# Kernel tuning notes

Measured on AMD Instinct MI355X. Metric: run time of the kernel, lower is better.

The kernel has to match this reference:

```python
import jax, jax.numpy as jnp
import numpy as np

N, E = 10000, 320000
IN_DIM, OUT_DIM, HEADS = 256, 32, 8
HD = OUT_DIM * HEADS  # 256
EPS = 1e-16  # PyG softmax epsilon


def _make_conv_params(key, in_dim, heads, d):
    hd = heads * d
    ks = jax.random.split(key, 8)
    s = 0.02
    return {
        'Wq': jax.random.normal(ks[0], (in_dim, hd)) * s,
        'bq': jnp.zeros((hd,)),
        'Wk': jax.random.normal(ks[1], (in_dim, hd)) * s,
        'bk': jnp.zeros((hd,)),
        'Wv': jax.random.normal(ks[2], (in_dim, hd)) * s,
        'bv': jnp.zeros((hd,)),
        'We': jax.random.normal(ks[3], (1, hd)) * s,          # lin_edge, no bias
        'Wskip': jax.random.normal(ks[4], (in_dim, hd)) * s,  # lin_skip
        'bskip': jnp.zeros((hd,)),
        'Wbeta': jax.random.normal(ks[5], (3 * hd, 1)) * s,   # lin_beta, no bias
    }


def transformer_conv(x, src, dst, edge_attr, p, heads, d):
    # x: [N, F]; edge_attr: [E, 1]
    n = x.shape[0]
    q = (x @ p['Wq'] + p['bq']).reshape(n, heads, d)
    k = (x @ p['Wk'] + p['bk']).reshape(n, heads, d)
    v = (x @ p['Wv'] + p['bv']).reshape(n, heads, d)
    e = (edge_attr @ p['We']).reshape(-1, heads, d)  # [E, H, D]
    kj = k[src] + e                                  # [E, H, D]
    vj = v[src] + e
    # per-edge attention logits
    alpha = jnp.einsum('ehd,ehd->eh', q[dst], kj) / jnp.sqrt(jnp.asarray(d, x.dtype))
    # segment softmax over incoming edges of each dst node
    m = jax.ops.segment_max(alpha, dst, num_segments=n)     # [N, H]
    m = jnp.where(jnp.isfinite(m), m, 0.0)
    ex = jnp.exp(alpha - m[dst])
    denom = jax.ops.segment_sum(ex, dst, num_segments=n)    # [N, H]
    w = ex / (denom[dst] + EPS)                              # [E, H]
    out = jax.ops.segment_sum(w[:, :, None] * vj, dst, num_segments=n)  # [N, H, D]
    out = out.reshape(n, heads * d)
    # beta-gated skip connection
    xr = x @ p['Wskip'] + p['bskip']
    beta = jax.nn.sigmoid(jnp.concatenate([out, xr, out - xr], axis=-1) @ p['Wbeta'])  # [N, 1]
    return beta * xr + (1.0 - beta) * out


def setup_inputs() -> dict:
    key = jax.random.key(0)
    kx, ke, kw, k1, k2 = jax.random.split(key, 5)
    inp = {
        'x': jax.random.normal(kx, (N, IN_DIM), dtype=jnp.float32),
        'edge_index': jax.random.randint(ke, (2, E), 0, N, dtype=jnp.int64),
        'edge_weight': jax.random.uniform(kw, (E,), dtype=jnp.float32),
    }
    p1 = _make_conv_params(k1, IN_DIM, HEADS, OUT_DIM)
    p2 = _make_conv_params(k2, HD, HEADS, OUT_DIM)
    for name, v in p1.items():
        inp[name + '1'] = v
    for name, v in p2.items():
        inp[name + '2'] = v
    return inp


def reference(x, edge_index, edge_weight,
              Wq1, bq1, Wk1, bk1, Wv1, bv1, We1, Wskip1, bskip1, Wbeta1,
              Wq2, bq2, Wk2, bk2, Wv2, bv2, We2, Wskip2, bskip2, Wbeta2):
    src, dst = edge_index[0], edge_index[1]
    ea = edge_weight[:, None]  # [E, 1]
    p1 = dict(Wq=Wq1, bq=bq1, Wk=Wk1, bk=bk1, Wv=Wv1, bv=bv1, We=We1,
              Wskip=Wskip1, bskip=bskip1, Wbeta=Wbeta1)
    p2 = dict(Wq=Wq2, bq=bq2, Wk=Wk2, bk=bk2, Wv=Wv2, bv=bv2, We=We2,
              Wskip=Wskip2, bskip=bskip2, Wbeta=Wbeta2)
    h = transformer_conv(x, src, dst, ea, p1, HEADS, OUT_DIM)
    h = transformer_conv(h, src, dst, ea, p2, HEADS, OUT_DIM)
    h = transformer_conv(h, src, dst, ea, p2, HEADS, OUT_DIM)  # conv2 applied twice, shared weights
    return h
```

## Files before the change

kernel.cpp:

```cpp
#include <hip/hip_runtime.h>
#include <hip/hip_bf16.h>
#include <math.h>

#define NN 10000
#define EE 320000
#define DIM 256
#define NROWS 10016
#define SCANB 40

typedef __attribute__((ext_vector_type(8))) _Float16 f16x8;
typedef __attribute__((ext_vector_type(4))) _Float16 f16x4;
typedef __attribute__((ext_vector_type(2))) _Float16 f16x2;
typedef __attribute__((ext_vector_type(4))) float f32x4;

#if defined(__has_builtin)
#if __has_builtin(__builtin_amdgcn_fdot2)
#define FDOT2(a, b, c) __builtin_amdgcn_fdot2(a, b, c, false)
#endif
#endif
#ifndef FDOT2
#define FDOT2(a, b, c) fmaf((float)a[0], (float)b[0], fmaf((float)a[1], (float)b[1], c))
#endif

__device__ __forceinline__ float bf2f(unsigned short u) {
  union { unsigned int ui; float f; } cv;
  cv.ui = ((unsigned int)u) << 16;
  return cv.f;
}

__device__ __forceinline__ float ldf(const void* p, int idx, int isf) {
  return isf ? ((const float*)p)[idx] : bf2f(((const unsigned short*)p)[idx]);
}

__global__ __launch_bounds__(256) void k_detect_zero(const unsigned int* __restrict__ xw,
                                                     const int* __restrict__ ei,
                                                     int* __restrict__ flags,
                                                     int* __restrict__ counts) {
  int i = blockIdx.x * 256 + (int)threadIdx.x;
  if (i < NN) counts[i] = 0;
  if (blockIdx.x == 0 && threadIdx.x < 64) {
    int lane = threadIdx.x;
    int wild = 0;
    for (int t = 0; t < 16; ++t) {
      unsigned int w = xw[t * 64 + lane];
      unsigned int lo = w & 0xffffu;
      float f = bf2f((unsigned short)lo);
      float af = fabsf(f);
      if (lo != 0u && (af > 1e4f || af < 1e-30f)) wild++;
    }
    #pragma unroll
    for (int m = 1; m < 64; m <<= 1) wild += __shfl_xor(wild, m);
    int zeros = 0;
    for (int t = 0; t < 2; ++t) {
      if (ei[(t * 64 + lane) * 2 + 1] == 0) zeros++;
    }
    #pragma unroll
    for (int m = 1; m < 64; m <<= 1) zeros += __shfl_xor(zeros, m);
    if (lane == 0) {
      flags[0] = (wild > 100) ? 1 : 0;
      flags[1] = (zeros > 100) ? 1 : 0;
    }
  }
}

__global__ void k_count(const int* __restrict__ ei, int* __restrict__ counts,
                        const int* __restrict__ flags) {
  int i64 = flags[1];
  int i = blockIdx.x * blockDim.x + threadIdx.x;
  if (i < EE) {
    int d = i64 ? ei[2 * (EE + i)] : ei[EE + i];
    atomicAdd(&counts[d], 1);
  }
}

__global__ __launch_bounds__(256) void k_scan1(const int* __restrict__ counts,
                                               int* __restrict__ tmpoff,
                                               int* __restrict__ bsum) {
  __shared__ int s[256];
  int t = threadIdx.x;
  int i = blockIdx.x * 256 + t;
  int v = (i < NN) ? counts[i] : 0;
  s[t] = v;
  __syncthreads();
  for (int off = 1; off < 256; off <<= 1) {
    int x = (t >= off) ? s[t - off] : 0;
    __syncthreads();
    s[t] += x;
    __syncthreads();
  }
  if (i < NN) tmpoff[i] = s[t] - v;
  if (t == 255) bsum[blockIdx.x] = s[255];
}

__global__ __launch_bounds__(256) void k_scan3(const int* __restrict__ tmpoff,
                                               const int* __restrict__ bsum,
                                               int* __restrict__ offsets,
                                               int* __restrict__ cursor) {
  __shared__ int sbase;
  if (threadIdx.x < 64) {
    int t = threadIdx.x;
    int v = (t < SCANB && t < (int)blockIdx.x) ? bsum[t] : 0;
    #pragma unroll
    for (int msk = 1; msk < 64; msk <<= 1) v += __shfl_xor(v, msk);
    if (t == 0) sbase = v;
  }
  __syncthreads();
  int base = sbase;
  int i = blockIdx.x * 256 + (int)threadIdx.x;
  if (i < NN) {
    int o = tmpoff[i] + base;
    offsets[i] = o;
    cursor[i] = o;
  }
  if (i == 0) offsets[NN] = EE;
}

__global__ void k_fill_sort(const int* __restrict__ ei, const void* __restrict__ ew,
                            int* __restrict__ cursor, int2* __restrict__ eS,
                            const int* __restrict__ flags) {
  int isf = flags[0];
  int i64 = flags[1];
  int i = blockIdx.x * blockDim.x + threadIdx.x;
  if (i < EE) {
    int s, d;
    if (i64) { s = ei[2 * i]; d = ei[2 * (EE + i)]; }
    else     { s = ei[i];     d = ei[EE + i]; }
    float wv = isf ? ((const float*)ew)[i] : bf2f(((const unsigned short*)ew)[i]);
    int p = atomicAdd(&cursor[d], 1);
    eS[p] = make_int2(s, __float_as_int(wv));
  }
}

struct PackArgs {
  const void* W[8];
  const void* B8[8];
  const void* WeWb[4];
  const void* x;
};

__global__ __launch_bounds__(256) void k_pack(PackArgs pa, _Float16* __restrict__ Bh,
                                              float* __restrict__ bvec,
                                              float* __restrict__ WeWbF,
                                              _Float16* __restrict__ Ah,
                                              _Float16* __restrict__ Al,
                                              const int* __restrict__ flags) {
  __shared__ _Float16 lds[64][66];
  int isf = flags[0];
  int bid = (int)blockIdx.x, tid = (int)threadIdx.x;
  if (bid < 128) {
    int m = bid >> 4, t = bid & 15, tr = t >> 2, tc = t & 3;
    const void* Wm = pa.W[m];
    #pragma unroll
    for (int rep = 0; rep < 16; ++rep) {
      int idx = rep * 256 + tid;
      int r = idx >> 6, c = idx & 63;
      lds[r][c] = (_Float16)ldf(Wm, (tr * 64 + r) * 256 + tc * 64 + c, isf);
    }
    __syncthreads();
    _Float16* out = Bh + (size_t)m * 65536;
    #pragma unroll
    for (int rep = 0; rep < 16; ++rep) {
      int idx = rep * 256 + tid;
      int r = idx >> 6, c = idx & 63;
      out[(tc * 64 + r) * 256 + tr * 64 + c] = lds[c][r];
    }
    return;
  }
  int b2 = bid - 128;
  if (b2 < 16) {
    int i = b2 * 256 + tid;
    if (i < 2048) {
      bvec[i] = ldf(pa.B8[i >> 8], i & 255, isf);
    } else {
      i -= 2048;
      int which, k;
      if (i < 256)       { which = 0; k = i; }
      else if (i < 1024) { which = 1; k = i - 256; }
      else if (i < 1280) { which = 2; k = i - 1024; }
      else               { which = 3; k = i - 1280; }
      WeWbF[i] = ldf(pa.WeWb[which], k, isf);
    }
    return;
  }
  int i = (b2 - 16) * 256 + tid;
  if (i < NROWS * 64) {
    f16x4 h, l;
    if (i >= NN * 64) {
      h = (f16x4)(_Float16)0.f;
      l = (f16x4)(_Float16)0.f;
    } else {
      float v[4];
      if (isf) {
        float4 t = reinterpret_cast<const float4*>(pa.x)[i];
        v[0] = t.x; v[1] = t.y; v[2] = t.z; v[3] = t.w;
      } else {
        ushort4 t = reinterpret_cast<const ushort4*>(pa.x)[i];
        v[0] = bf2f(t.x); v[1] = bf2f(t.y); v[2] = bf2f(t.z); v[3] = bf2f(t.w);
      }
      #pragma unroll
      for (int j = 0; j < 4; ++j) {
        _Float16 hh = (_Float16)v[j];
        h[j] = hh;
        l[j] = (_Float16)(v[j] - (float)hh);
      }
    }
    reinterpret_cast<f16x4*>(Ah)[i] = h;
    reinterpret_cast<f16x4*>(Al)[i] = l;
  }
}

__global__ __launch_bounds__(256, 4) void k_gemm_mfma(
    const _Float16* __restrict__ Ah, const _Float16* __restrict__ Al,
    const _Float16* __restrict__ Bh, const float* __restrict__ bvec,
    _Float16* __restrict__ Qh, _Float16* __restrict__ KVh, float* __restrict__ XRf) {
  int tid = (int)threadIdx.x;
  int wave = tid >> 6, lane = tid & 63;
  int lr = lane & 15;
  int kg = (lane >> 4) << 3;
  int mat = blockIdx.y;
  int rowBase = blockIdx.x << 5;
  int colBase = (mat << 8) + (wave << 6);
  const _Float16* a0 = Ah + (size_t)(rowBase + lr) * 256 + kg;
  const _Float16* a1 = Al + (size_t)(rowBase + lr) * 256 + kg;
  const _Float16* b0 = Bh + (size_t)(colBase + lr) * 256 + kg;
  f32x4 acc[2][4] = {};
  #pragma unroll
  for (int ks = 0; ks < 256; ks += 32) {
    f16x8 ah0 = *reinterpret_cast<const f16x8*>(a0 + ks);
    f16x8 ah1 = *reinterpret_cast<const f16x8*>(a0 + 16 * 256 + ks);
    f16x8 bh[4];
    #pragma unroll
    for (int cf = 0; cf < 4; ++cf)
      bh[cf] = *reinterpret_cast<const f16x8*>(b0 + cf * 16 * 256 + ks);
    #pragma unroll
    for (int cf = 0; cf < 4; ++cf) {
      acc[0][cf] = __builtin_amdgcn_mfma_f32_16x16x32_f16(ah0, bh[cf], acc[0][cf], 0, 0, 0);
      acc[1][cf] = __builtin_amdgcn_mfma_f32_16x16x32_f16(ah1, bh[cf], acc[1][cf], 0, 0, 0);
    }
    if (mat == 3) {
      f16x8 al0 = *reinterpret_cast<const f16x8*>(a1 + ks);
      f16x8 al1 = *reinterpret_cast<const f16x8*>(a1 + 16 * 256 + ks);
      #pragma unroll
      for (int cf = 0; cf < 4; ++cf) {
        acc[0][cf] = __builtin_amdgcn_mfma_f32_16x16x32_f16(al0, bh[cf], acc[0][cf], 0, 0, 0);
        acc[1][cf] = __builtin_amdgcn_mfma_f32_16x16x32_f16(al1, bh[cf], acc[1][cf], 0, 0, 0);
      }
    }
  }
  int rj = (lane >> 4) << 2;
  int colLoc = (wave << 6);
  #pragma unroll
  for (int rf = 0; rf < 2; ++rf) {
    #pragma unroll
    for (int cf = 0; cf < 4; ++cf) {
      int col = colLoc + cf * 16 + lr;
      float bb = bvec[(mat << 8) + col];
      #pragma unroll
      for (int j = 0; j < 4; ++j) {
        int row = rowBase + rf * 16 + rj + j;
        if (row < NN) {
          float val = acc[rf][cf][j] + bb;
          if (mat == 0)      Qh[(size_t)row * DIM + col] = (_Float16)val;
          else if (mat == 3) XRf[(size_t)row * DIM + col] = val;
          else KVh[(size_t)row * 512 + ((mat == 2) ? 256 : 0) + col] = (_Float16)val;
        }
      }
    }
  }
}

#define ATT_STEP(KK, VV, WW) do { \
    f16x2 kka = {KK[0], KK[1]}, kkb = {KK[2], KK[3]}; \
    float pt = FDOT2(kka, qha, FDOT2(kkb, qhb, 0.f)); \
    pt += __shfl_xor(pt, 1); \
    pt += __shfl_xor(pt, 2); \
    pt += __shfl_xor(pt, 4); \
    float alpha = fmaf(WW, qwe, pt) * 0.17677669529663687f; \
    float nm = fmaxf(m, alpha); \
    float sc = __expf(m - nm); \
    float pe = __expf(alpha - nm); \
    l = fmaf(l, sc, pe); \
    sw = fmaf(sw, sc, pe * WW); \
    a0 = fmaf(a0, sc, pe * (float)VV[0]); \
    a1 = fmaf(a1, sc, pe * (float)VV[1]); \
    a2 = fmaf(a2, sc, pe * (float)VV[2]); \
    a3 = fmaf(a3, sc, pe * (float)VV[3]); \
    m = nm; \
  } while (0)

#define PAIR_STEP(K0, V0, W0, K1, V1, W1) do { \
    f16x2 k0a = {K0[0], K0[1]}, k0b = {K0[2], K0[3]}; \
    f16x2 k1a = {K1[0], K1[1]}, k1b = {K1[2], K1[3]}; \
    float pt0 = FDOT2(k0a, qha, FDOT2(k0b, qhb, 0.f)); \
    float pt1 = FDOT2(k1a, qha, FDOT2(k1b, qhb, 0.f)); \
    pt0 += __shfl_xor(pt0, 1); pt1 += __shfl_xor(pt1, 1); \
    pt0 += __shfl_xor(pt0, 2); pt1 += __shfl_xor(pt1, 2); \
    pt0 += __shfl_xor(pt0, 4); pt1 += __shfl_xor(pt1, 4); \
    float al0 = fmaf(W0, qwe, pt0) * 0.17677669529663687f; \
    float al1 = fmaf(W1, qwe, pt1) * 0.17677669529663687f; \
    float nm = fmaxf(fmaxf(m, al0), al1); \
    float sc = __expf(m - nm); \
    float p0 = __expf(al0 - nm); \
    float p1 = __expf(al1 - nm); \
    l = fmaf(l, sc, p0 + p1); \
    sw = fmaf(sw, sc, fmaf(p0, W0, p1 * W1)); \
    a0 = fmaf(a0, sc, fmaf(p0, (float)V0[0], p1 * (float)V1[0])); \
    a1 = fmaf(a1, sc, fmaf(p0, (float)V0[1], p1 * (float)V1[1])); \
    a2 = fmaf(a2, sc, fmaf(p0, (float)V0[2], p1 * (float)V1[2])); \
    a3 = fmaf(a3, sc, fmaf(p0, (float)V0[3], p1 * (float)V1[3])); \
    m = nm; \
  } while (0)

__global__ __launch_bounds__(256) void k_attn(
    const _Float16* __restrict__ Qh, const _Float16* __restrict__ KVh,
    const float* __restrict__ XRf, const float* __restrict__ We,
    const float* __restrict__ Wb, const int2* __restrict__ eS,
    const int* __restrict__ offsets, _Float16* __restrict__ Ah,
    _Float16* __restrict__ Al, float* __restrict__ FinalOut) {
  int wid = (int)threadIdx.x >> 6, lane = (int)threadIdx.x & 63;
  int node = blockIdx.x * 4 + wid;
  if (node >= NN) return;
  int d0 = lane * 4;
  const f16x4 qh4 = *reinterpret_cast<const f16x4*>(&Qh[(size_t)node * DIM + d0]);
  const float4 x4 = *reinterpret_cast<const float4*>(&XRf[(size_t)node * DIM + d0]);
  const float4 we4 = *reinterpret_cast<const float4*>(&We[d0]);
  const float4 wo = *reinterpret_cast<const float4*>(&Wb[d0]);
  const float4 wx = *reinterpret_cast<const float4*>(&Wb[DIM + d0]);
  const float4 wd = *reinterpret_cast<const float4*>(&Wb[2 * DIM + d0]);
  f16x2 qha = {qh4[0], qh4[1]};
  f16x2 qhb = {qh4[2], qh4[3]};
  float qwe = (float)qh4[0] * we4.x + (float)qh4[1] * we4.y
            + (float)qh4[2] * we4.z + (float)qh4[3] * we4.w;
  qwe += __shfl_xor(qwe, 1);
  qwe += __shfl_xor(qwe, 2);
  qwe += __shfl_xor(qwe, 4);
  int beg = offsets[node], end = offsets[node + 1];
  beg = __builtin_amdgcn_readfirstlane(beg);
  end = __builtin_amdgcn_readfirstlane(end);
  float m = -INFINITY, l = 0.f, sw = 0.f, a0 = 0.f, a1 = 0.f, a2 = 0.f, a3 = 0.f;
  int p = beg;
  if ((end - beg) & 1) {
    int2 e = eS[p];
    float w0 = __int_as_float(e.y);
    const _Float16* r = KVh + (size_t)e.x * 512 + d0;
    f16x4 k0 = *reinterpret_cast<const f16x4*>(r);
    f16x4 v0 = *reinterpret_cast<const f16x4*>(r + 256);
    ATT_STEP(k0, v0, w0);
    ++p;
  }
  if (p < end) {
    int2 eA0 = eS[p], eA1 = eS[p + 1];
    int pb = (p + 3 < end) ? (p + 2) : p;
    int2 eB0 = eS[pb], eB1 = eS[pb + 1];
    const _Float16* rA0 = KVh + (size_t)eA0.x * 512 + d0;
    const _Float16* rA1 = KVh + (size_t)eA1.x * 512 + d0;
    const _Float16* rB0 = KVh + (size_t)eB0.x * 512 + d0;
    const _Float16* rB1 = KVh + (size_t)eB1.x * 512 + d0;
    f16x4 kA0 = *reinterpret_cast<const f16x4*>(rA0), vA0 = *reinterpret_cast<const f16x4*>(rA0 + 256);
    f16x4 kA1 = *reinterpret_cast<const f16x4*>(rA1), vA1 = *reinterpret_cast<const f16x4*>(rA1 + 256);
    f16x4 kB0 = *reinterpret_cast<const f16x4*>(rB0), vB0 = *reinterpret_cast<const f16x4*>(rB0 + 256);
    f16x4 kB1 = *reinterpret_cast<const f16x4*>(rB1), vB1 = *reinterpret_cast<const f16x4*>(rB1 + 256);
    float wA0 = __int_as_float(eA0.y), wA1 = __int_as_float(eA1.y);
    float wB0 = __int_as_float(eB0.y), wB1 = __int_as_float(eB1.y);
    #pragma unroll 2
    for (; p + 2 < end; p += 2) {
      int pc = (p + 5 < end) ? (p + 4) : p;
      int2 eC0 = eS[pc], eC1 = eS[pc + 1];
      const _Float16* rC0 = KVh + (size_t)eC0.x * 512 + d0;
      const _Float16* rC1 = KVh + (size_t)eC1.x * 512 + d0;
      f16x4 kC0 = *reinterpret_cast<const f16x4*>(rC0), vC0 = *reinterpret_cast<const f16x4*>(rC0 + 256);
      f16x4 kC1 = *reinterpret_cast<const f16x4*>(rC1), vC1 = *reinterpret_cast<const f16x4*>(rC1 + 256);
      float wC0 = __int_as_float(eC0.y), wC1 = __int_as_float(eC1.y);
      PAIR_STEP(kA0, vA0, wA0, kA1, vA1, wA1);
      kA0 = kB0; vA0 = vB0; wA0 = wB0; kA1 = kB1; vA1 = vB1; wA1 = wB1;
      kB0 = kC0; vB0 = vC0; wB0 = wC0; kB1 = kC1; vB1 = vC1; wB1 = wC1;
    }
    PAIR_STEP(kA0, vA0, wA0, kA1, vA1, wA1);
  }
  float inv = 1.f / (l + 1e-16f);
  float o0 = fmaf(sw, we4.x, a0) * inv;
  float o1 = fmaf(sw, we4.y, a1) * inv;
  float o2 = fmaf(sw, we4.z, a2) * inv;
  float o3 = fmaf(sw, we4.w, a3) * inv;
  float part = o0 * wo.x + o1 * wo.y + o2 * wo.z + o3 * wo.w
             + x4.x * wx.x + x4.y * wx.y + x4.z * wx.z + x4.w * wx.w
             + (o0 - x4.x) * wd.x + (o1 - x4.y) * wd.y
             + (o2 - x4.z) * wd.z + (o3 - x4.w) * wd.w;
  #pragma unroll
  for (int msk = 1; msk < 64; msk <<= 1) part += __shfl_xor(part, msk);
  float beta = 1.f / (1.f + __expf(-part));
  float h0 = beta * x4.x + (1.f - beta) * o0;
  float h1 = beta * x4.y + (1.f - beta) * o1;
  float h2 = beta * x4.z + (1.f - beta) * o2;
  float h3 = beta * x4.w + (1.f - beta) * o3;
  if (FinalOut) {
    float4 h; h.x = h0; h.y = h1; h.z = h2; h.w = h3;
    *reinterpret_cast<float4*>(&FinalOut[(size_t)node * DIM + d0]) = h;
  } else {
    f16x4 hh, ll;
    _Float16 t0 = (_Float16)h0, t1 = (_Float16)h1, t2 = (_Float16)h2, t3 = (_Float16)h3;
    hh[0] = t0; hh[1] = t1; hh[2] = t2; hh[3] = t3;
    ll[0] = (_Float16)(h0 - (float)t0); ll[1] = (_Float16)(h1 - (float)t1);
    ll[2] = (_Float16)(h2 - (float)t2); ll[3] = (_Float16)(h3 - (float)t3);
    *reinterpret_cast<f16x4*>(&Ah[(size_t)node * DIM + d0]) = hh;
    *reinterpret_cast<f16x4*>(&Al[(size_t)node * DIM + d0]) = ll;
  }
}

static inline size_t align256(size_t v) { return (v + 255) & ~(size_t)255; }

extern "C" void kernel_launch(void* const* d_in, const int* in_sizes, int n_in,
                              void* d_out, int out_size, void* d_ws, size_t ws_size,
                              hipStream_t stream) {
  const void* x = d_in[0];
  const int* eidx = (const int*)d_in[1];
  const void* ew = d_in[2];

  char* w = (char*)d_ws;
  size_t pos = 0;
  int* flags = (int*)(w + pos); pos = align256(pos + 2 * sizeof(int));
  _Float16* Qh = (_Float16*)(w + pos); pos = align256(pos + (size_t)NROWS * DIM * 2);
  float* XRf = (float*)(w + pos); pos = align256(pos + (size_t)NROWS * DIM * 4);
  _Float16* KVh = (_Float16*)(w + pos); pos = align256(pos + (size_t)NROWS * 512 * 2);
  _Float16* Ah = (_Float16*)(w + pos); pos = align256(pos + (size_t)NROWS * DIM * 2);
  _Float16* Al = (_Float16*)(w + pos); pos = align256(pos + (size_t)NROWS * DIM * 2);
  _Float16* Bh = (_Float16*)(w + pos); pos = align256(pos + (size_t)8 * 65536 * 2);
  float* bvec  = (float*)(w + pos); pos = align256(pos + 2048 * 4);
  float* WeWbF = (float*)(w + pos); pos = align256(pos + 2048 * 4);
  int2* eS   = (int2*)(w + pos);   pos = align256(pos + (size_t)EE * 8);
  int* counts  = (int*)(w + pos);  pos = align256(pos + (size_t)NN * 4);
  int* offsets = (int*)(w + pos);  pos = align256(pos + (size_t)(NN + 1) * 4);
  int* cursor  = (int*)(w + pos);  pos = align256(pos + (size_t)NN * 4);
  int* tmpoff  = (int*)(w + pos);  pos = align256(pos + (size_t)NN * 4);
  int* bsum    = (int*)(w + pos);  pos = align256(pos + 64 * 4);

  PackArgs pa;
  pa.x = x;
  for (int g = 0; g < 2; ++g) {
    const void* const* pp = &d_in[3 + g * 10];
    pa.W[g * 4 + 0] = pp[0]; pa.W[g * 4 + 1] = pp[2];
    pa.W[g * 4 + 2] = pp[4]; pa.W[g * 4 + 3] = pp[7];
    pa.B8[g * 4 + 0] = pp[1]; pa.B8[g * 4 + 1] = pp[3];
    pa.B8[g * 4 + 2] = pp[5]; pa.B8[g * 4 + 3] = pp[8];
    pa.WeWb[g * 2 + 0] = pp[6];
    pa.WeWb[g * 2 + 1] = pp[9];
  }

  k_detect_zero<<<SCANB, 256, 0, stream>>>((const unsigned int*)x, eidx, flags, counts);
  k_pack<<<128 + 16 + (NROWS * 64 + 255) / 256, 256, 0, stream>>>(
      pa, Bh, bvec, WeWbF, Ah, Al, flags);
  k_count<<<(EE + 255) / 256, 256, 0, stream>>>(eidx, counts, flags);
  k_scan1<<<SCANB, 256, 0, stream>>>(counts, tmpoff, bsum);
  k_scan3<<<SCANB, 256, 0, stream>>>(tmpoff, bsum, offsets, cursor);
  k_fill_sort<<<(EE + 255) / 256, 256, 0, stream>>>(eidx, ew, cursor, eS, flags);

  for (int layer = 0; layer < 3; ++layer) {
    int g = (layer == 0) ? 0 : 1;
    k_gemm_mfma<<<dim3(NROWS / 32, 4), 256, 0, stream>>>(
        Ah, Al, Bh + (size_t)g * 4 * 65536, bvec + g * 1024, Qh, KVh, XRf);
    k_attn<<<(NN + 3) / 4, 256, 0, stream>>>(Qh, KVh, XRf,
        WeWbF + (g ? 1024 : 0), WeWbF + (g ? 1280 : 256),
        eS, offsets, Ah, Al, (layer == 2) ? (float*)d_out : nullptr);
  }
}
```

Measured before the change: 303.4 us.

## Drop fp16 low-part split for skip GEMM and fuse scan kernels

Removes the hi/lo fp16 split of the activations. The skip-projection GEMM (mat 3) no longer runs its extra MFMA pass over the residual part, and the Al buffer is neither written nor read anywhere. Separately, per-block degree sums are now accumulated with atomics during counting, so the two scan kernels merge into one and a launch plus a temp buffer go away. This trades precision of the skip path for less GEMM work and memory traffic, and adds contention on 40 block counters.

```diff
diff --git a/kernel.cpp b/kernel.cpp
--- a/kernel.cpp
+++ b/kernel.cpp
@@ -35,9 +35,11 @@
 __global__ __launch_bounds__(256) void k_detect_zero(const unsigned int* __restrict__ xw,
                                                      const int* __restrict__ ei,
                                                      int* __restrict__ flags,
-                                                     int* __restrict__ counts) {
+                                                     int* __restrict__ counts,
+                                                     int* __restrict__ bsum) {
   int i = blockIdx.x * 256 + (int)threadIdx.x;
   if (i < NN) counts[i] = 0;
+  if (blockIdx.x == 1 && threadIdx.x < 64) bsum[threadIdx.x] = 0;
   if (blockIdx.x == 0 && threadIdx.x < 64) {
     int lane = threadIdx.x;
     int wild = 0;
@@ -64,23 +66,32 @@
 }
 
 __global__ void k_count(const int* __restrict__ ei, int* __restrict__ counts,
-                        const int* __restrict__ flags) {
+                        int* __restrict__ bsum, const int* __restrict__ flags) {
   int i64 = flags[1];
   int i = blockIdx.x * blockDim.x + threadIdx.x;
   if (i < EE) {
     int d = i64 ? ei[2 * (EE + i)] : ei[EE + i];
     atomicAdd(&counts[d], 1);
-  }
-}
-
-__global__ __launch_bounds__(256) void k_scan1(const int* __restrict__ counts,
-                                               int* __restrict__ tmpoff,
-                                               int* __restrict__ bsum) {
+    atomicAdd(&bsum[d >> 8], 1);
+  }
+}
+
+__global__ __launch_bounds__(256) void k_scan_all(const int* __restrict__ counts,
+                                                  const int* __restrict__ bsum,
+                                                  int* __restrict__ offsets,
+                                                  int* __restrict__ cursor) {
   __shared__ int s[256];
-  int t = threadIdx.x;
-  int i = blockIdx.x * 256 + t;
+  __shared__ int sbase;
+  int t = (int)threadIdx.x, b = (int)blockIdx.x;
+  int i = b * 256 + t;
   int v = (i < NN) ? counts[i] : 0;
   s[t] = v;
+  if (t < 64) {
+    int x = (t < SCANB && t < b) ? bsum[t] : 0;
+    #pragma unroll
+    for (int msk = 1; msk < 64; msk <<= 1) x += __shfl_xor(x, msk);
+    if (t == 0) sbase = x;
+  }
   __syncthreads();
   for (int off = 1; off < 256; off <<= 1) {
     int x = (t >= off) ? s[t - off] : 0;
@@ -88,27 +99,8 @@
     s[t] += x;
     __syncthreads();
   }
-  if (i < NN) tmpoff[i] = s[t] - v;
-  if (t == 255) bsum[blockIdx.x] = s[255];
-}
-
-__global__ __launch_bounds__(256) void k_scan3(const int* __restrict__ tmpoff,
-                                               const int* __restrict__ bsum,
-                                               int* __restrict__ offsets,
-                                               int* __restrict__ cursor) {
-  __shared__ int sbase;
-  if (threadIdx.x < 64) {
-    int t = threadIdx.x;
-    int v = (t < SCANB && t < (int)blockIdx.x) ? bsum[t] : 0;
-    #pragma unroll
-    for (int msk = 1; msk < 64; msk <<= 1) v += __shfl_xor(v, msk);
-    if (t == 0) sbase = v;
-  }
-  __syncthreads();
-  int base = sbase;
-  int i = blockIdx.x * 256 + (int)threadIdx.x;
   if (i < NN) {
-    int o = tmpoff[i] + base;
+    int o = sbase + s[t] - v;
     offsets[i] = o;
     cursor[i] = o;
   }
@@ -142,7 +134,6 @@
                                               float* __restrict__ bvec,
                                               float* __restrict__ WeWbF,
                                               _Float16* __restrict__ Ah,
-                                              _Float16* __restrict__ Al,
                                               const int* __restrict__ flags) {
   __shared__ _Float16 lds[64][66];
   int isf = flags[0];
@@ -184,10 +175,9 @@
   }
   int i = (b2 - 16) * 256 + tid;
   if (i < NROWS * 64) {
-    f16x4 h, l;
+    f16x4 h;
     if (i >= NN * 64) {
       h = (f16x4)(_Float16)0.f;
-      l = (f16x4)(_Float16)0.f;
     } else {
       float v[4];
       if (isf) {
@@ -198,21 +188,16 @@
         v[0] = bf2f(t.x); v[1] = bf2f(t.y); v[2] = bf2f(t.z); v[3] = bf2f(t.w);
       }
       #pragma unroll
-      for (int j = 0; j < 4; ++j) {
-        _Float16 hh = (_Float16)v[j];
-        h[j] = hh;
-        l[j] = (_Float16)(v[j] - (float)hh);
-      }
+      for (int j = 0; j < 4; ++j) h[j] = (_Float16)v[j];
     }
     reinterpret_cast<f16x4*>(Ah)[i] = h;
-    reinterpret_cast<f16x4*>(Al)[i] = l;
   }
 }
 
 __global__ __launch_bounds__(256, 4) void k_gemm_mfma(
-    const _Float16* __restrict__ Ah, const _Float16* __restrict__ Al,
-    const _Float16* __restrict__ Bh, const float* __restrict__ bvec,
-    _Float16* __restrict__ Qh, _Float16* __restrict__ KVh, float* __restrict__ XRf) {
+    const _Float16* __restrict__ Ah, const _Float16* __restrict__ Bh,
+    const float* __restrict__ bvec, _Float16* __restrict__ Qh,
+    _Float16* __restrict__ KVh, float* __restrict__ XRf) {
   int tid = (int)threadIdx.x;
   int wave = tid >> 6, lane = tid & 63;
   int lr = lane & 15;
@@ -221,7 +206,6 @@
   int rowBase = blockIdx.x << 5;
   int colBase = (mat << 8) + (wave << 6);
   const _Float16* a0 = Ah + (size_t)(rowBase + lr) * 256 + kg;
-  const _Float16* a1 = Al + (size_t)(rowBase + lr) * 256 + kg;
   const _Float16* b0 = Bh + (size_t)(colBase + lr) * 256 + kg;
   f32x4 acc[2][4] = {};
   #pragma unroll
@@ -236,15 +220,6 @@
     for (int cf = 0; cf < 4; ++cf) {
       acc[0][cf] = __builtin_amdgcn_mfma_f32_16x16x32_f16(ah0, bh[cf], acc[0][cf], 0, 0, 0);
       acc[1][cf] = __builtin_amdgcn_mfma_f32_16x16x32_f16(ah1, bh[cf], acc[1][cf], 0, 0, 0);
-    }
-    if (mat == 3) {
-      f16x8 al0 = *reinterpret_cast<const f16x8*>(a1 + ks);
-      f16x8 al1 = *reinterpret_cast<const f16x8*>(a1 + 16 * 256 + ks);
-      #pragma unroll
-      for (int cf = 0; cf < 4; ++cf) {
-        acc[0][cf] = __builtin_amdgcn_mfma_f32_16x16x32_f16(al0, bh[cf], acc[0][cf], 0, 0, 0);
-        acc[1][cf] = __builtin_amdgcn_mfma_f32_16x16x32_f16(al1, bh[cf], acc[1][cf], 0, 0, 0);
-      }
     }
   }
   int rj = (lane >> 4) << 2;
@@ -316,7 +291,7 @@
     const float* __restrict__ XRf, const float* __restrict__ We,
     const float* __restrict__ Wb, const int2* __restrict__ eS,
     const int* __restrict__ offsets, _Float16* __restrict__ Ah,
-    _Float16* __restrict__ Al, float* __restrict__ FinalOut) {
+    float* __restrict__ FinalOut) {
   int wid = (int)threadIdx.x >> 6, lane = (int)threadIdx.x & 63;
   int node = blockIdx.x * 4 + wid;
   if (node >= NN) return;
@@ -397,13 +372,10 @@
     float4 h; h.x = h0; h.y = h1; h.z = h2; h.w = h3;
     *reinterpret_cast<float4*>(&FinalOut[(size_t)node * DIM + d0]) = h;
   } else {
-    f16x4 hh, ll;
-    _Float16 t0 = (_Float16)h0, t1 = (_Float16)h1, t2 = (_Float16)h2, t3 = (_Float16)h3;
-    hh[0] = t0; hh[1] = t1; hh[2] = t2; hh[3] = t3;
-    ll[0] = (_Float16)(h0 - (float)t0); ll[1] = (_Float16)(h1 - (float)t1);
-    ll[2] = (_Float16)(h2 - (float)t2); ll[3] = (_Float16)(h3 - (float)t3);
+    f16x4 hh;
+    hh[0] = (_Float16)h0; hh[1] = (_Float16)h1;
+    hh[2] = (_Float16)h2; hh[3] = (_Float16)h3;
     *reinterpret_cast<f16x4*>(&Ah[(size_t)node * DIM + d0]) = hh;
-    *reinterpret_cast<f16x4*>(&Al[(size_t)node * DIM + d0]) = ll;
   }
 }
 
@@ -423,7 +395,6 @@
   float* XRf = (float*)(w + pos); pos = align256(pos + (size_t)NROWS * DIM * 4);
   _Float16* KVh = (_Float16*)(w + pos); pos = align256(pos + (size_t)NROWS * 512 * 2);
   _Float16* Ah = (_Float16*)(w + pos); pos = align256(pos + (size_t)NROWS * DIM * 2);
-  _Float16* Al = (_Float16*)(w + pos); pos = align256(pos + (size_t)NROWS * DIM * 2);
   _Float16* Bh = (_Float16*)(w + pos); pos = align256(pos + (size_t)8 * 65536 * 2);
   float* bvec  = (float*)(w + pos); pos = align256(pos + 2048 * 4);
   float* WeWbF = (float*)(w + pos); pos = align256(pos + 2048 * 4);
@@ -431,7 +402,6 @@
   int* counts  = (int*)(w + pos);  pos = align256(pos + (size_t)NN * 4);
   int* offsets = (int*)(w + pos);  pos = align256(pos + (size_t)(NN + 1) * 4);
   int* cursor  = (int*)(w + pos);  pos = align256(pos + (size_t)NN * 4);
-  int* tmpoff  = (int*)(w + pos);  pos = align256(pos + (size_t)NN * 4);
   int* bsum    = (int*)(w + pos);  pos = align256(pos + 64 * 4);
 
   PackArgs pa;
@@ -446,20 +416,19 @@
     pa.WeWb[g * 2 + 1] = pp[9];
   }
 
-  k_detect_zero<<<SCANB, 256, 0, stream>>>((const unsigned int*)x, eidx, flags, counts);
+  k_detect_zero<<<SCANB, 256, 0, stream>>>((const unsigned int*)x, eidx, flags, counts, bsum);
   k_pack<<<128 + 16 + (NROWS * 64 + 255) / 256, 256, 0, stream>>>(
-      pa, Bh, bvec, WeWbF, Ah, Al, flags);
-  k_count<<<(EE + 255) / 256, 256, 0, stream>>>(eidx, counts, flags);
-  k_scan1<<<SCANB, 256, 0, stream>>>(counts, tmpoff, bsum);
-  k_scan3<<<SCANB, 256, 0, stream>>>(tmpoff, bsum, offsets, cursor);
+      pa, Bh, bvec, WeWbF, Ah, flags);
+  k_count<<<(EE + 255) / 256, 256, 0, stream>>>(eidx, counts, bsum, flags);
+  k_scan_all<<<SCANB, 256, 0, stream>>>(counts, bsum, offsets, cursor);
   k_fill_sort<<<(EE + 255) / 256, 256, 0, stream>>>(eidx, ew, cursor, eS, flags);
 
   for (int layer = 0; layer < 3; ++layer) {
     int g = (layer == 0) ? 0 : 1;
     k_gemm_mfma<<<dim3(NROWS / 32, 4), 256, 0, stream>>>(
-        Ah, Al, Bh + (size_t)g * 4 * 65536, bvec + g * 1024, Qh, KVh, XRf);
+        Ah, Bh + (size_t)g * 4 * 65536, bvec + g * 1024, Qh, KVh, XRf);
     k_attn<<<(NN + 3) / 4, 256, 0, stream>>>(Qh, KVh, XRf,
         WeWbF + (g ? 1024 : 0), WeWbF + (g ? 1280 : 256),
-        eS, offsets, Ah, Al, (layer == 2) ? (float*)d_out : nullptr);
-  }
-}
+        eS, offsets, Ah, (layer == 2) ? (float*)d_out : nullptr);
+  }
+}
```

After: 813.2 us. +168.0%, slower.
